# Optimization experiments

Hardware: AMD Instinct MI355X
Metric: run time of the kernel (lower is better)

Reference implementation:

```python
import jax, jax.numpy as jnp
import numpy as np

TAU = 20.0            # membrane time constant
TAU_ADAPT = 20.0      # threshold adaptation time constant
BETA = 1.8            # adaptation strength (n_regular=0 -> all neurons adaptive)
DAMPENING = 1.0       # surrogate-gradient dampening
REF_PERIOD = 2.0      # refractory period (steps)
THR = 0.03            # base threshold
INTERNAL_CURRENT = 0.0


@jax.custom_vjp
def spike_fn(v_sc):
    # Heaviside forward; triangular pseudo-derivative backward.
    return (v_sc > 0.0).astype(v_sc.dtype)

def _spike_fwd(v_sc):
    return spike_fn(v_sc), v_sc

def _spike_bwd(v_sc, g):
    # triangular pseudo-derivative: dampening * max(0, 1 - |v_sc|) (sharpness=1)
    return (g * DAMPENING * jnp.maximum(0.0, 1.0 - jnp.abs(v_sc)),)

spike_fn.defvjp(_spike_fwd, _spike_bwd)


def setup_inputs() -> dict:
    key = jax.random.key(0)
    kx, kin, krec = jax.random.split(key, 3)
    B, T, NI, N = 128, 500, 256, 256
    x = jax.random.normal(kx, (B, T, NI), dtype=jnp.float32)
    w_in = jax.random.normal(kin, (NI, N), dtype=jnp.float32) / np.float32(np.sqrt(NI))
    w_rec = jax.random.normal(krec, (N, N), dtype=jnp.float32) / np.float32(np.sqrt(N))
    zeros = jnp.zeros((B, N), dtype=jnp.float32)
    return {"x": x, "w_in": w_in, "w_rec": w_rec,
            "z0": zeros, "v0": zeros, "a0": zeros, "lsd0": zeros}


def _lsnn_scan(x, w_in, w_rec, z0, v0, a0, lsd0):
    n = w_rec.shape[0]
    mask = 1.0 - jnp.eye(n, dtype=x.dtype)          # zero out self-connections
    w_rec_m = mask * w_rec
    decay_v = jnp.exp(jnp.asarray(-1.0 / TAU, x.dtype))
    decay_a = jnp.exp(jnp.asarray(-1.0 / TAU_ADAPT, x.dtype))
    beta_vec = jnp.full((n,), BETA, dtype=x.dtype)  # n_regular = 0

    def step(carry, x_t):
        old_z, old_v, old_a, lsd = carry
        # currents: external + masked recurrent + constant internal
        i_in = x_t @ w_in + old_z @ w_rec_m + INTERNAL_CURRENT
        # adaptive threshold dynamics
        new_a = decay_a * old_a + (1.0 - decay_a) * old_z
        thr = THR + new_a * beta_vec
        # voltage dynamics with reset current
        i_reset = -thr * old_z
        new_v = decay_v * old_v + (1.0 - decay_v) * i_in + i_reset
        # surrogate spike
        v_sc = (new_v - thr) / thr
        z = spike_fn(v_sc)
        # refractoriness
        non_ref = (lsd >= REF_PERIOD).astype(x.dtype)
        z = non_ref * z
        new_lsd = (lsd + 1.0) * (1.0 - z)
        return (z, new_v, new_a, new_lsd), (z, new_v, thr, v_sc)

    x_t_first = jnp.swapaxes(x, 0, 1)               # [T, B, n_in]
    _, (zs, vs, thrs, vscs) = jax.lax.scan(step, (z0, v0, a0, lsd0), x_t_first)
    # stack the 4 per-step outputs -> [4, T, B, N]
    return jnp.stack([zs, vs, thrs, vscs], axis=0)


def reference(x, w_in, w_rec, z0, v0, a0, lsd0):
    return _lsnn_scan(x, w_in, w_rec, z0, v0, a0, lsd0)
```

## Files before the change

### kernel.cpp

```cpp
#include <hip/hip_runtime.h>

#define T_STEPS 500
#define N_NEUR  256
#define N_IN    256
#define N_BATCH 128

__global__ __launch_bounds__(256) void xw_gemm_kernel(
    const float* __restrict__ A,
    const float* __restrict__ W,
    float* __restrict__ C)
{
    __shared__ float As[16][129];
    __shared__ float Bs[16][68];
    const int tid = threadIdx.x;
    const int bm  = blockIdx.x;
    const int bn  = blockIdx.y;
    const int ty  = tid >> 4;
    const int tx  = tid & 15;
    const int arow  = tid >> 1;
    const int akoff = (tid & 1) * 8;
    const int brow  = tid >> 4;
    const int bcol  = (tid & 15) * 4;
    const float* Ab = A + (size_t)bm * 128 * 256;

    float acc[8][4];
#pragma unroll
    for (int i = 0; i < 8; ++i)
#pragma unroll
        for (int j = 0; j < 4; ++j) acc[i][j] = 0.f;

    for (int k0 = 0; k0 < 256; k0 += 16) {
        float4 av0 = *(const float4*)(Ab + (size_t)arow * 256 + k0 + akoff);
        float4 av1 = *(const float4*)(Ab + (size_t)arow * 256 + k0 + akoff + 4);
        float4 bv  = *(const float4*)(W + (size_t)(k0 + brow) * 256 + bn * 64 + bcol);
        __syncthreads();
        As[akoff + 0][arow] = av0.x; As[akoff + 1][arow] = av0.y;
        As[akoff + 2][arow] = av0.z; As[akoff + 3][arow] = av0.w;
        As[akoff + 4][arow] = av1.x; As[akoff + 5][arow] = av1.y;
        As[akoff + 6][arow] = av1.z; As[akoff + 7][arow] = av1.w;
        *(float4*)&Bs[brow][bcol] = bv;
        __syncthreads();
#pragma unroll
        for (int kk = 0; kk < 16; ++kk) {
            float a[8], b[4];
#pragma unroll
            for (int i = 0; i < 8; ++i) a[i] = As[kk][ty * 8 + i];
#pragma unroll
            for (int j = 0; j < 4; ++j) b[j] = Bs[kk][tx * 4 + j];
#pragma unroll
            for (int i = 0; i < 8; ++i)
#pragma unroll
                for (int j = 0; j < 4; ++j)
                    acc[i][j] += a[i] * b[j];
        }
    }
    const int crow = bm * 128 + ty * 8;
    const int ccol = bn * 64 + tx * 4;
#pragma unroll
    for (int i = 0; i < 8; ++i) {
        float4 v = make_float4(acc[i][0], acc[i][1], acc[i][2], acc[i][3]);
        *(float4*)(C + (size_t)(crow + i) * 256 + ccol) = v;
    }
}

__global__ void prep_wrec_kernel(const float* __restrict__ w_rec,
                                 float* __restrict__ wz)
{
    int i = blockIdx.x * 256 + threadIdx.x;
    if (i < 256 * 256) {
        int r = i >> 8, c = i & 255;
        wz[i] = (r == c) ? 0.f : w_rec[i];
    } else {
        wz[i] = 0.f;
    }
}

__global__ __launch_bounds__(1024) void lsnn_scan3_kernel(
    const float* __restrict__ xw,
    const float* __restrict__ wz,
    const float* __restrict__ z0, const float* __restrict__ v0,
    const float* __restrict__ a0, const float* __restrict__ lsd0,
    float* __restrict__ out)
{
    const int b   = blockIdx.x;
    const int t0  = threadIdx.x;
    const int n   = t0 >> 2;
    const int seg = t0 & 3;

    __shared__ __align__(16) float zsh[2][4][72];

    const float dv   = (float)0.9512294245007140018;
    const float omdv = 1.0f - dv;

    float w[64];
    {
        const float* wc = wz + (size_t)seg * 64 * N_NEUR + n;
#pragma unroll
        for (int k = 0; k < 64; ++k) w[k] = wc[(size_t)k * N_NEUR];
    }

    const int bn = b * N_NEUR + n;
    float z   = z0[bn];
    float v   = v0[bn];
    float a   = a0[bn];
    float lsd = lsd0[bn];

    if (seg == 0) zsh[0][n >> 6][n & 63] = z;
    __syncthreads();

    float x_next = xw[((size_t)b * T_STEPS) * N_NEUR + n];
    const size_t PL = (size_t)T_STEPS * N_BATCH * N_NEUR;

    for (int t = 0; t < T_STEPS; ++t) {
        float x_cur = x_next;
        {
            int tn = (t + 1 < T_STEPS) ? t + 1 : t;
            x_next = xw[((size_t)b * T_STEPS + tn) * N_NEUR + n];
        }
        const int rb = t & 1;

        const float* zr = &zsh[rb][seg][0];
        float p = 0.f;
#pragma unroll
        for (int k4 = 0; k4 < 16; ++k4) {
            float4 zv = *(const float4*)(zr + 4 * k4);
            p = fmaf(zv.x, w[4 * k4 + 0], p);
            p = fmaf(zv.y, w[4 * k4 + 1], p);
            p = fmaf(zv.z, w[4 * k4 + 2], p);
            p = fmaf(zv.w, w[4 * k4 + 3], p);
        }

        const int pi = __float_as_int(p);
        const float q0 = __int_as_float(__builtin_amdgcn_mov_dpp(pi, 0x00, 0xF, 0xF, true));
        const float q1 = __int_as_float(__builtin_amdgcn_mov_dpp(pi, 0x55, 0xF, 0xF, true));
        const float q2 = __int_as_float(__builtin_amdgcn_mov_dpp(pi, 0xAA, 0xF, 0xF, true));
        const float q3 = __int_as_float(__builtin_amdgcn_mov_dpp(pi, 0xFF, 0xF, 0xF, true));
        float i_rec = ((q0 + q1) + q2) + q3;

        float i_in  = x_cur + i_rec;
        float new_a = dv * a + omdv * z;
        float thr   = 0.03f + new_a * 1.8f;
        float new_v = dv * v + omdv * i_in - thr * z;
        float v_sc  = (new_v - thr) / thr;
        float zs    = (v_sc > 0.f) ? 1.f : 0.f;
        zs          = (lsd >= 2.0f) ? zs : 0.f;
        float new_lsd = (lsd + 1.f) * (1.f - zs);

        size_t o = (size_t)t * (N_BATCH * N_NEUR) + (size_t)b * N_NEUR + n;
        float outv = (seg == 0) ? zs : (seg == 1) ? new_v
                   : (seg == 2) ? thr : v_sc;
        __builtin_nontemporal_store(outv, out + o + (size_t)seg * PL);

        v = new_v; a = new_a; lsd = new_lsd; z = zs;

        if (seg == 0) zsh[rb ^ 1][n >> 6][n & 63] = zs;
        __syncthreads();
    }
}

template <bool USE_XW>
__global__ __launch_bounds__(256) void lsnn_scan_kernel(
    const float* __restrict__ xin,
    const float* __restrict__ w_in,
    const float* __restrict__ w_rec,
    const float* __restrict__ z0, const float* __restrict__ v0,
    const float* __restrict__ a0, const float* __restrict__ lsd0,
    float* __restrict__ out)
{
    const int b    = blockIdx.x;
    const int n    = threadIdx.x;
    const int lane = n & 63;
    const int wid  = n >> 6;

    __shared__ int   cnt4[4];
    __shared__ int   act[256];
    __shared__ float xsh[256];

    const float dv   = (float)0.9512294245007140018;
    const float omdv = 1.0f - dv;

    const int base_bn = b * N_NEUR + n;
    float z   = z0[base_bn];
    float v   = v0[base_bn];
    float a   = a0[base_bn];
    float lsd = lsd0[base_bn];

    act[n] = 0;
    {
        unsigned long long wm = __ballot(z != 0.f);
        if (lane == 0) cnt4[wid] = __popcll(wm);
        if (z != 0.f) {
            int pos = __popcll(wm & ((1ull << lane) - 1ull));
            act[wid * 64 + pos] = n;
        }
        if (!USE_XW) xsh[n] = xin[((size_t)b * T_STEPS) * N_IN + n];
    }
    __syncthreads();

    float x_next = USE_XW ? xin[((size_t)b * T_STEPS) * N_NEUR + n] : 0.f;

    for (int t = 0; t < T_STEPS; ++t) {
        float x_cur = x_next;
        if (USE_XW) {
            int tn = (t + 1 < T_STEPS) ? t + 1 : t;
            x_next = xin[((size_t)b * T_STEPS + tn) * N_NEUR + n];
        }
        const int cs0 = cnt4[0], cs1 = cnt4[1], cs2 = cnt4[2], cs3 = cnt4[3];
        int mx = max(max(cs0, cs1), max(cs2, cs3));
        float r0 = 0.f, r1 = 0.f, r2 = 0.f, r3 = 0.f;
        for (int i0 = 0; i0 < mx; i0 += 8) {
            float wv[4][8];
            bool  ok[4][8];
#pragma unroll
            for (int s = 0; s < 4; ++s) {
                const int cs = (s == 0) ? cs0 : (s == 1) ? cs1 : (s == 2) ? cs2 : cs3;
#pragma unroll
                for (int j = 0; j < 8; ++j) {
                    int ii = i0 + j;
                    int m  = act[s * 64 + (ii < cs ? ii : 0)] & 255;
                    wv[s][j] = w_rec[m * N_NEUR + n];
                    ok[s][j] = (ii < cs) && (m != n);
                }
            }
#pragma unroll
            for (int j = 0; j < 8; ++j) r0 += ok[0][j] ? wv[0][j] : 0.f;
#pragma unroll
            for (int j = 0; j < 8; ++j) r1 += ok[1][j] ? wv[1][j] : 0.f;
#pragma unroll
            for (int j = 0; j < 8; ++j) r2 += ok[2][j] ? wv[2][j] : 0.f;
#pragma unroll
            for (int j = 0; j < 8; ++j) r3 += ok[3][j] ? wv[3][j] : 0.f;
        }
        float i_rec = ((r0 + r1) + r2) + r3;

        float xdot;
        if (USE_XW) {
            xdot = x_cur;
        } else {
            float s = 0.f;
#pragma unroll 8
            for (int m = 0; m < N_IN; ++m) s += xsh[m] * w_in[m * N_NEUR + n];
            xdot = s;
        }
        float i_in = xdot + i_rec;

        float new_a = dv * a + omdv * z;
        float thr   = 0.03f + new_a * 1.8f;
        float new_v = dv * v + omdv * i_in - thr * z;
        float v_sc  = (new_v - thr) / thr;
        float zs    = (v_sc > 0.f) ? 1.f : 0.f;
        zs          = (lsd >= 2.0f) ? zs : 0.f;
        float new_lsd = (lsd + 1.f) * (1.f - zs);

        const size_t PL = (size_t)T_STEPS * N_BATCH * N_NEUR;
        size_t o = (size_t)t * (N_BATCH * N_NEUR) + (size_t)b * N_NEUR + n;
        out[o]          = zs;
        out[o + PL]     = new_v;
        out[o + 2 * PL] = thr;
        out[o + 3 * PL] = v_sc;

        v = new_v; a = new_a; lsd = new_lsd; z = zs;

        __syncthreads();
        unsigned long long wm = __ballot(zs != 0.f);
        if (lane == 0) cnt4[wid] = __popcll(wm);
        if (zs != 0.f) {
            int pos = __popcll(wm & ((1ull << lane) - 1ull));
            act[wid * 64 + pos] = n;
        }
        if (!USE_XW && (t + 1 < T_STEPS))
            xsh[n] = xin[((size_t)b * T_STEPS + t + 1) * N_IN + n];
        __syncthreads();
    }
}

extern "C" void kernel_launch(void* const* d_in, const int* in_sizes, int n_in,
                              void* d_out, int out_size, void* d_ws, size_t ws_size,
                              hipStream_t stream) {
    const float* x     = (const float*)d_in[0];
    const float* w_in  = (const float*)d_in[1];
    const float* w_rec = (const float*)d_in[2];
    const float* z0    = (const float*)d_in[3];
    const float* v0    = (const float*)d_in[4];
    const float* a0    = (const float*)d_in[5];
    const float* lsd0  = (const float*)d_in[6];
    float* out = (float*)d_out;

    const size_t xw_bytes = (size_t)N_BATCH * T_STEPS * N_NEUR * sizeof(float);
    const size_t wz_bytes = (size_t)257 * 256 * sizeof(float);

    if (ws_size >= xw_bytes + wz_bytes) {
        float* xw = (float*)d_ws;
        float* wz = (float*)((char*)d_ws + xw_bytes);
        prep_wrec_kernel<<<257, 256, 0, stream>>>(w_rec, wz);
        dim3 grid(500, 4, 1);
        xw_gemm_kernel<<<grid, 256, 0, stream>>>(x, w_in, xw);
        lsnn_scan3_kernel<<<N_BATCH, 1024, 0, stream>>>(
            xw, wz, z0, v0, a0, lsd0, out);
    } else if (ws_size >= xw_bytes) {
        float* xw = (float*)d_ws;
        dim3 grid(500, 4, 1);
        xw_gemm_kernel<<<grid, 256, 0, stream>>>(x, w_in, xw);
        lsnn_scan_kernel<true><<<N_BATCH, 256, 0, stream>>>(
            xw, nullptr, w_rec, z0, v0, a0, lsd0, out);
    } else {
        lsnn_scan_kernel<false><<<N_BATCH, 256, 0, stream>>>(
            x, w_in, w_rec, z0, v0, a0, lsd0, out);
    }
}
```

Baseline: 748.8 us.

## Double-buffer input GEMM with 128x128 tiles and lighten scan barrier

```diff
diff --git a/kernel.cpp b/kernel.cpp
--- a/kernel.cpp
+++ b/kernel.cpp
@@ -5,13 +5,15 @@
 #define N_IN    256
 #define N_BATCH 128
 
-__global__ __launch_bounds__(256) void xw_gemm_kernel(
+#define BPOS(c) ((c) + (((c) >> 4) << 2))
+
+__global__ __launch_bounds__(256) void xw_gemm5_kernel(
     const float* __restrict__ A,
     const float* __restrict__ W,
     float* __restrict__ C)
 {
-    __shared__ float As[16][129];
-    __shared__ float Bs[16][68];
+    __shared__ float As[2][16][132];
+    __shared__ float Bs[2][16][160];
     const int tid = threadIdx.x;
     const int bm  = blockIdx.x;
     const int bn  = blockIdx.y;
@@ -20,46 +22,72 @@
     const int arow  = tid >> 1;
     const int akoff = (tid & 1) * 8;
     const int brow  = tid >> 4;
-    const int bcol  = (tid & 15) * 4;
+    const int bcol  = (tid & 15) * 8;
     const float* Ab = A + (size_t)bm * 128 * 256;
 
-    float acc[8][4];
+    float acc[8][8];
 #pragma unroll
     for (int i = 0; i < 8; ++i)
 #pragma unroll
-        for (int j = 0; j < 4; ++j) acc[i][j] = 0.f;
-
-    for (int k0 = 0; k0 < 256; k0 += 16) {
-        float4 av0 = *(const float4*)(Ab + (size_t)arow * 256 + k0 + akoff);
-        float4 av1 = *(const float4*)(Ab + (size_t)arow * 256 + k0 + akoff + 4);
-        float4 bv  = *(const float4*)(W + (size_t)(k0 + brow) * 256 + bn * 64 + bcol);
+        for (int j = 0; j < 8; ++j) acc[i][j] = 0.f;
+
+    {
+        float4 av0 = *(const float4*)(Ab + (size_t)arow * 256 + akoff);
+        float4 av1 = *(const float4*)(Ab + (size_t)arow * 256 + akoff + 4);
+        float4 bv0 = *(const float4*)(W + (size_t)brow * 256 + bn * 128 + bcol);
+        float4 bv1 = *(const float4*)(W + (size_t)brow * 256 + bn * 128 + bcol + 4);
+        As[0][akoff + 0][arow] = av0.x; As[0][akoff + 1][arow] = av0.y;
+        As[0][akoff + 2][arow] = av0.z; As[0][akoff + 3][arow] = av0.w;
+        As[0][akoff + 4][arow] = av1.x; As[0][akoff + 5][arow] = av1.y;
+        As[0][akoff + 6][arow] = av1.z; As[0][akoff + 7][arow] = av1.w;
+        *(float4*)&Bs[0][brow][BPOS(bcol)]     = bv0;
+        *(float4*)&Bs[0][brow][BPOS(bcol) + 4] = bv1;
+    }
+    __syncthreads();
+
+    for (int it = 0; it < 16; ++it) {
+        const int cur = it & 1;
+        float4 av0, av1, bv0, bv1;
+        const bool pf = (it + 1 < 16);
+        if (pf) {
+            const int k0 = (it + 1) * 16;
+            av0 = *(const float4*)(Ab + (size_t)arow * 256 + k0 + akoff);
+            av1 = *(const float4*)(Ab + (size_t)arow * 256 + k0 + akoff + 4);
+            bv0 = *(const float4*)(W + (size_t)(k0 + brow) * 256 + bn * 128 + bcol);
+            bv1 = *(const float4*)(W + (size_t)(k0 + brow) * 256 + bn * 128 + bcol + 4);
+        }
+#pragma unroll
+        for (int kk = 0; kk < 16; ++kk) {
+            float a[8], b[8];
+#pragma unroll
+            for (int i = 0; i < 8; ++i) a[i] = As[cur][kk][ty * 8 + i];
+#pragma unroll
+            for (int j = 0; j < 8; ++j) b[j] = Bs[cur][kk][BPOS(tx * 8) + j];
+#pragma unroll
+            for (int i = 0; i < 8; ++i)
+#pragma unroll
+                for (int j = 0; j < 8; ++j)
+                    acc[i][j] += a[i] * b[j];
+        }
+        if (pf) {
+            As[cur ^ 1][akoff + 0][arow] = av0.x; As[cur ^ 1][akoff + 1][arow] = av0.y;
+            As[cur ^ 1][akoff + 2][arow] = av0.z; As[cur ^ 1][akoff + 3][arow] = av0.w;
+            As[cur ^ 1][akoff + 4][arow] = av1.x; As[cur ^ 1][akoff + 5][arow] = av1.y;
+            As[cur ^ 1][akoff + 6][arow] = av1.z; As[cur ^ 1][akoff + 7][arow] = av1.w;
+            *(float4*)&Bs[cur ^ 1][brow][BPOS(bcol)]     = bv0;
+            *(float4*)&Bs[cur ^ 1][brow][BPOS(bcol) + 4] = bv1;
+        }
         __syncthreads();
-        As[akoff + 0][arow] = av0.x; As[akoff + 1][arow] = av0.y;
-        As[akoff + 2][arow] = av0.z; As[akoff + 3][arow] = av0.w;
-        As[akoff + 4][arow] = av1.x; As[akoff + 5][arow] = av1.y;
-        As[akoff + 6][arow] = av1.z; As[akoff + 7][arow] = av1.w;
-        *(float4*)&Bs[brow][bcol] = bv;
-        __syncthreads();
-#pragma unroll
-        for (int kk = 0; kk < 16; ++kk) {
-            float a[8], b[4];
-#pragma unroll
-            for (int i = 0; i < 8; ++i) a[i] = As[kk][ty * 8 + i];
-#pragma unroll
-            for (int j = 0; j < 4; ++j) b[j] = Bs[kk][tx * 4 + j];
-#pragma unroll
-            for (int i = 0; i < 8; ++i)
-#pragma unroll
-                for (int j = 0; j < 4; ++j)
-                    acc[i][j] += a[i] * b[j];
-        }
-    }
+    }
+
     const int crow = bm * 128 + ty * 8;
-    const int ccol = bn * 64 + tx * 4;
+    const int ccol = bn * 128 + tx * 8;
 #pragma unroll
     for (int i = 0; i < 8; ++i) {
-        float4 v = make_float4(acc[i][0], acc[i][1], acc[i][2], acc[i][3]);
-        *(float4*)(C + (size_t)(crow + i) * 256 + ccol) = v;
+        float4 v0 = make_float4(acc[i][0], acc[i][1], acc[i][2], acc[i][3]);
+        float4 v1 = make_float4(acc[i][4], acc[i][5], acc[i][6], acc[i][7]);
+        *(float4*)(C + (size_t)(crow + i) * 256 + ccol)     = v0;
+        *(float4*)(C + (size_t)(crow + i) * 256 + ccol + 4) = v1;
     }
 }
 
@@ -154,7 +182,9 @@
         v = new_v; a = new_a; lsd = new_lsd; z = zs;
 
         if (seg == 0) zsh[rb ^ 1][n >> 6][n & 63] = zs;
-        __syncthreads();
+        asm volatile("s_waitcnt lgkmcnt(0)" ::: "memory");
+        __builtin_amdgcn_s_barrier();
+        asm volatile("" ::: "memory");
     }
 }
 
@@ -212,14 +242,14 @@
             float wv[4][8];
             bool  ok[4][8];
 #pragma unroll
-            for (int s = 0; s < 4; ++s) {
-                const int cs = (s == 0) ? cs0 : (s == 1) ? cs1 : (s == 2) ? cs2 : cs3;
+            for (int sgi = 0; sgi < 4; ++sgi) {
+                const int cs = (sgi == 0) ? cs0 : (sgi == 1) ? cs1 : (sgi == 2) ? cs2 : cs3;
 #pragma unroll
                 for (int j = 0; j < 8; ++j) {
                     int ii = i0 + j;
-                    int m  = act[s * 64 + (ii < cs ? ii : 0)] & 255;
-                    wv[s][j] = w_rec[m * N_NEUR + n];
-                    ok[s][j] = (ii < cs) && (m != n);
+                    int m  = act[sgi * 64 + (ii < cs ? ii : 0)] & 255;
+                    wv[sgi][j] = w_rec[m * N_NEUR + n];
+                    ok[sgi][j] = (ii < cs) && (m != n);
                 }
             }
 #pragma unroll
@@ -237,10 +267,10 @@
         if (USE_XW) {
             xdot = x_cur;
         } else {
-            float s = 0.f;
+            float sum = 0.f;
 #pragma unroll 8
-            for (int m = 0; m < N_IN; ++m) s += xsh[m] * w_in[m * N_NEUR + n];
-            xdot = s;
+            for (int m = 0; m < N_IN; ++m) sum += xsh[m] * w_in[m * N_NEUR + n];
+            xdot = sum;
         }
         float i_in = xdot + i_rec;
 
@@ -293,14 +323,14 @@
         float* xw = (float*)d_ws;
         float* wz = (float*)((char*)d_ws + xw_bytes);
         prep_wrec_kernel<<<257, 256, 0, stream>>>(w_rec, wz);
-        dim3 grid(500, 4, 1);
-        xw_gemm_kernel<<<grid, 256, 0, stream>>>(x, w_in, xw);
+        dim3 grid(500, 2, 1);
+        xw_gemm5_kernel<<<grid, 256, 0, stream>>>(x, w_in, xw);
         lsnn_scan3_kernel<<<N_BATCH, 1024, 0, stream>>>(
             xw, wz, z0, v0, a0, lsd0, out);
     } else if (ws_size >= xw_bytes) {
         float* xw = (float*)d_ws;
-        dim3 grid(500, 4, 1);
-        xw_gemm_kernel<<<grid, 256, 0, stream>>>(x, w_in, xw);
+        dim3 grid(500, 2, 1);
+        xw_gemm5_kernel<<<grid, 256, 0, stream>>>(x, w_in, xw);
         lsnn_scan_kernel<true><<<N_BATCH, 256, 0, stream>>>(
             xw, nullptr, w_rec, z0, v0, a0, lsd0, out);
     } else {
```

Measured after the change: 793.9 us. 6.0% more time.
